# Kernel tuning notes

Measured on AMD Instinct MI355X. Metric: run time of the kernel, lower is better.

## Reference

```python
import jax, jax.numpy as jnp
import numpy as np

N_NODES = 50000
N_EDGES = 800000
IN_F = 256
HID = 64          # hidden_features; GAT layers output 2*HID = 128
OUT_F = 2
NUM_GRAPHS = 32
NEG_SLOPE = 0.2   # PyG GATConv default


def setup_inputs() -> dict:
    key = jax.random.key(0)
    ks = jax.random.split(key, 16)
    g = 2 * HID
    def glorot(k, shape):
        fan_in = shape[0] if len(shape) > 1 else shape[0]
        return jax.random.normal(k, shape, dtype=jnp.float32) / np.sqrt(fan_in)
    return {
        "x": jax.random.normal(ks[0], (N_NODES, IN_F), dtype=jnp.float32),
        "edge_index": jax.random.randint(ks[1], (2, N_EDGES), 0, N_NODES, dtype=jnp.int64),
        "batch": jnp.sort(jax.random.randint(ks[2], (N_NODES,), 0, NUM_GRAPHS, dtype=jnp.int64)),
        "W1": glorot(ks[3], (IN_F, g)),
        "as1": glorot(ks[4], (g,)),
        "ad1": glorot(ks[5], (g,)),
        "b1": jnp.zeros((g,), jnp.float32),
        "W2": glorot(ks[6], (g, g)),
        "as2": glorot(ks[7], (g,)),
        "ad2": glorot(ks[8], (g,)),
        "b2": jnp.zeros((g,), jnp.float32),
        "lw1": glorot(ks[9], (g, HID)),
        "lb1": jnp.zeros((HID,), jnp.float32),
        "lw2": glorot(ks[10], (HID, OUT_F)),
        "lb2": jnp.zeros((OUT_F,), jnp.float32),
    }


def _gat_conv(x, W, a_src, a_dst, bias, src, dst, n):
    # Single-head PyG GATConv: linear -> per-edge LeakyReLU attention logits ->
    # softmax over incoming edges per destination -> weighted scatter-sum.
    h = x @ W                                   # [N, F]
    es = h @ a_src                              # [N] source attention terms
    ed = h @ a_dst                              # [N] destination attention terms
    e = jax.nn.leaky_relu(es[src] + ed[dst], NEG_SLOPE)   # [E]
    m = jax.ops.segment_max(e, dst, num_segments=n)
    m = jnp.where(jnp.isfinite(m), m, 0.0)      # guard empty segments
    ex = jnp.exp(e - m[dst])
    den = jax.ops.segment_sum(ex, dst, num_segments=n)
    alpha = ex / (den[dst] + 1e-16)             # PyG softmax epsilon
    out = jax.ops.segment_sum(alpha[:, None] * h[src], dst, num_segments=n)
    return out + bias


def reference(x, edge_index, batch, W1, as1, ad1, b1, W2, as2, ad2, b2, lw1, lb1, lw2, lb2):
    n = x.shape[0]
    loops = jnp.arange(n, dtype=edge_index.dtype)
    src = jnp.concatenate([edge_index[0], loops])   # add_self_loops=True (PyG default)
    dst = jnp.concatenate([edge_index[1], loops])

    h = jax.nn.selu(_gat_conv(x, W1, as1, ad1, b1, src, dst, n))
    h = jax.nn.selu(_gat_conv(h, W2, as2, ad2, b2, src, dst, n))

    # global_mean_pool over graph-batch vector
    sums = jax.ops.segment_sum(h, batch, num_segments=NUM_GRAPHS)
    cnts = jax.ops.segment_sum(jnp.ones((n,), h.dtype), batch, num_segments=NUM_GRAPHS)
    pooled = sums / jnp.maximum(cnts, 1.0)[:, None]     # [B, 2*HID]

    z = jax.nn.selu(pooled)
    z = jax.nn.selu(z @ lw1 + lb1)
    z = z @ lw2 + lb2
    return jax.nn.log_softmax(z, axis=-1)
```

## Files before the change

kernel.cpp:

```cpp
#include <hip/hip_runtime.h>
#include <hip/hip_bf16.h>
#include <math.h>

#define N_NODES 50000
#define N_EDGES 800000
#define ET (N_EDGES + N_NODES)
#define IN_F 256
#define G 128
#define NHID 64
#define NGRAPH 32
#define NBUCK ((N_NODES + 255) / 256)
#define CAP 8192
#define POOL_NODES 64
#define EPB 4096
#define NBA ((ET + EPB - 1) / EPB)

typedef __hip_bfloat16 bf16;
typedef unsigned short ushort;
typedef __attribute__((ext_vector_type(8))) short short8;
typedef __attribute__((ext_vector_type(4))) float f32x4;

__device__ __forceinline__ float bf2f(ushort u) {
    union { unsigned u; float f; } c; c.u = ((unsigned)u) << 16; return c.f;
}
__device__ __forceinline__ ushort f2bf(float f) {
    unsigned u = __float_as_uint(f);
    u += 0x7FFFu + ((u >> 16) & 1u);
    return (ushort)(u >> 16);
}
__device__ __forceinline__ float ldf(const void* p, long i, int f32) {
    return f32 ? ((const float*)p)[i] : bf2f(((const ushort*)p)[i]);
}
__device__ __forceinline__ int ldi(const void* p, long i, int i64) {
    return i64 ? (int)((const long long*)p)[i] : ((const int*)p)[i];
}

__device__ __forceinline__ float selu_f(float x) {
    const float sc = 1.0507009873554805f, al = 1.6732632423543772f;
    return x > 0.f ? sc * x : sc * al * expm1f(x);
}

typedef const __attribute__((address_space(1))) void gas_void;
typedef __attribute__((address_space(3))) void las_void;
__device__ __forceinline__ void stage16(const void* g, void* l) {
    __builtin_amdgcn_global_load_lds((gas_void*)g, (las_void*)l, 16, 0, 0);
}

__global__ void detect_kernel(const void* x, const void* ei, int* flags,
                              int* bcur, float* gsum, float* gcnt) {
    int l = threadIdx.x;
    for (int k = l; k < NBUCK; k += 64) bcur[k] = 0;
    for (int k = l; k < NGRAPH * G; k += 64) gsum[k] = 0.f;
    if (l < NGRAPH) gcnt[l] = 0.f;
    const unsigned* xu = (const unsigned*)x;
    const long NW = (long)N_NODES * IN_F / 2;
    long stride = NW / 1024;
    int sane = 0;
    for (int k = l; k < 1024; k += 64) {
        unsigned u = xu[(long)k * stride];
        unsigned e = (u >> 23) & 0xFF;
        if (u == 0u || (e >= 100 && e <= 140)) sane++;
    }
    const unsigned* wu = (const unsigned*)ei;
    int nz = 0;
    for (int k = l; k < 1024; k += 64) {
        long j = ((long)k * 1562) | 1;
        nz += (wu[j] != 0u);
    }
    for (int off = 32; off; off >>= 1) {
        sane += __shfl_xor(sane, off);
        nz   += __shfl_xor(nz, off);
    }
    if (l == 0) {
        flags[0] = (sane >= 512) ? 1 : 0;
        flags[1] = (nz < 16) ? 1 : 0;
    }
}

__device__ __forceinline__ void edge_sd(const void* __restrict__ ei, int e, int i64,
                                        int& s, int& d) {
    if (e < N_EDGES) {
        s = ldi(ei, e, i64);
        d = ldi(ei, (long)N_EDGES + e, i64);
        s = min(max(s, 0), N_NODES - 1);
        d = min(max(d, 0), N_NODES - 1);
    } else {
        s = d = e - N_EDGES;
    }
}


__global__ __launch_bounds__(256) void binA_kernel(
    const void* __restrict__ ei, int* __restrict__ bcur, unsigned* __restrict__ pairs,
    const int* __restrict__ flags) {
    __shared__ int cnt[256], lofs[256], pcur[256], gbase[256];
    __shared__ unsigned stage[EPB];
    int t = threadIdx.x;
    int e0 = blockIdx.x * EPB;
    int nE = min(EPB, ET - e0);
    int i64 = flags[1];
    int sj[EPB / 256], dj[EPB / 256];
    cnt[t] = 0;
    __syncthreads();
#pragma unroll
    for (int j = 0; j < EPB / 256; j++) {
        int idx = j * 256 + t;
        if (idx < nE) {
            edge_sd(ei, e0 + idx, i64, sj[j], dj[j]);
            atomicAdd(&cnt[dj[j] >> 8], 1);
        } else dj[j] = -1;
    }
    __syncthreads();
    lofs[t] = cnt[t];
    for (int off = 1; off < 256; off <<= 1) {
        __syncthreads();
        int v = (t >= off) ? lofs[t - off] : 0;
        __syncthreads();
        lofs[t] += v;
    }
    __syncthreads();
    int excl = lofs[t] - cnt[t];
    __syncthreads();
    lofs[t] = excl;
    pcur[t] = excl;
    __syncthreads();
    if (t < NBUCK && cnt[t]) gbase[t] = atomicAdd(&bcur[t], cnt[t]);
    __syncthreads();
#pragma unroll
    for (int j = 0; j < EPB / 256; j++) {
        if (dj[j] >= 0) {
            int b = dj[j] >> 8;
            int lp = atomicAdd(&pcur[b], 1);
            stage[lp] = (unsigned)sj[j] | ((unsigned)(dj[j] & 255) << 16) |
                        ((unsigned)b << 24);
        }
    }
    __syncthreads();
    for (int i = t; i < nE; i += 256) {
        unsigned p = stage[i];
        int b = p >> 24;
        int idx = gbase[b] + i - lofs[b];
        if (idx < CAP)
            pairs[(size_t)b * CAP + idx] = p;
    }
}

__global__ __launch_bounds__(256) void binB_kernel(
    const unsigned* __restrict__ pairs, const int* __restrict__ bcur,
    int2* __restrict__ rowse, ushort* __restrict__ srcs) {
    __shared__ int cnt[256], cur[256];
    int b = blockIdx.x, t = threadIdx.x;
    int base = b * CAP;
    int n = min(bcur[b], CAP);
    cnt[t] = 0;
    __syncthreads();
    for (int i = t; i < n; i += 256)
        atomicAdd(&cnt[(pairs[base + i] >> 16) & 255], 1);
    __syncthreads();
    cur[t] = cnt[t];
    for (int off = 1; off < 256; off <<= 1) {
        __syncthreads();
        int v = (t >= off) ? cur[t - off] : 0;
        __syncthreads();
        cur[t] += v;
    }
    __syncthreads();
    int excl = cur[t] - cnt[t];
    __syncthreads();
    cur[t] = base + excl;
    int node = b * 256 + t;
    if (node < N_NODES) rowse[node] = make_int2(base + excl, base + excl + cnt[t]);
    __syncthreads();
    for (int i = t; i < n; i += 256) {
        unsigned p = pairs[base + i];
        int pos = atomicAdd(&cur[(p >> 16) & 255], 1);
        srcs[pos] = (ushort)(p & 0xFFFFu);
    }
}

__global__ void wt_kernel(const void* __restrict__ W1, const void* __restrict__ W2,
                          ushort* __restrict__ wt1, ushort* __restrict__ wt2,
                          const int* __restrict__ flags) {
    int i = blockIdx.x * 256 + threadIdx.x;
    int f32 = flags[0];
    const void* W; ushort* wt; int idx;
    if (i < IN_F * G) { W = W1; wt = wt1; idx = i; }
    else if (i < IN_F * G + G * G) { W = W2; wt = wt2; idx = i - IN_F * G; }
    else return;
    int k = idx >> 7, n = idx & (G - 1);
    float w = ldf(W, idx, f32);
    ushort h = f2bf(w);
    ushort lo = f2bf(w - bf2f(h));
    int c = k >> 5, q = (k >> 3) & 3, j = k & 7;
    int nt = n >> 4, n16 = n & 15;
    int lane = q * 16 + n16;
    size_t base = ((size_t)c * 16 + nt * 2) * 512 + lane * 8 + j;
    wt[base] = h;
    wt[base + 512] = lo;
}

template <int K, bool AF32>
__device__ __forceinline__ void gemm_body(
    const void* __restrict__ A, const ushort* __restrict__ wt,
    unsigned* __restrict__ H2, const int* __restrict__ flags,
    const void* __restrict__ aS, const void* __restrict__ aD,
    float2* __restrict__ es2, short8* sB8) {
    constexpr int NC = K / 32;
    int wave = threadIdx.x >> 6, lane = threadIdx.x & 63;
    int quad = lane >> 4, n16 = lane & 15;
    int rb = blockIdx.x * 64 + wave * 16;
    int rowa = min(rb + n16, N_NODES - 1);
    f32x4 acc[8];
#pragma unroll
    for (int t = 0; t < 8; t++) acc[t] = (f32x4){0.f, 0.f, 0.f, 0.f};

    for (int c = 0; c < NC; c++) {
#pragma unroll
        for (int i = 0; i < 4; i++) {
            int fw = wave * 4 + i;
            stage16(wt + ((size_t)c * 16 + fw) * 512 + lane * 8, &sB8[fw * 64]);
        }
        float av[8];
        if (AF32) {
            const float* ap = (const float*)A + (size_t)rowa * K + c * 32 + quad * 8;
            f32x4 a0 = *(const f32x4*)ap;
            f32x4 a1 = *(const f32x4*)(ap + 4);
#pragma unroll
            for (int j = 0; j < 4; j++) { av[j] = a0[j]; av[j + 4] = a1[j]; }
        } else {
            const ushort* ap = (const ushort*)A + (size_t)rowa * K + c * 32 + quad * 8;
#pragma unroll
            for (int j = 0; j < 8; j++) av[j] = bf2f(ap[j]);
        }
        short8 ahi, alo;
#pragma unroll
        for (int j = 0; j < 8; j++) {
            ushort h = f2bf(av[j]);
            ahi[j] = (short)h;
            alo[j] = (short)f2bf(av[j] - bf2f(h));
        }
        __syncthreads();
#pragma unroll
        for (int nt = 0; nt < 8; nt++) {
            short8 bh = sB8[(nt * 2 + 0) * 64 + lane];
            short8 bl = sB8[(nt * 2 + 1) * 64 + lane];
            acc[nt] = __builtin_amdgcn_mfma_f32_16x16x32_bf16(ahi, bh, acc[nt], 0, 0, 0);
            acc[nt] = __builtin_amdgcn_mfma_f32_16x16x32_bf16(ahi, bl, acc[nt], 0, 0, 0);
            acc[nt] = __builtin_amdgcn_mfma_f32_16x16x32_bf16(alo, bh, acc[nt], 0, 0, 0);
        }
        __syncthreads();
    }

    int f32 = flags[0];
    float asv[8], adv[8];
#pragma unroll
    for (int nt = 0; nt < 8; nt++) {
        asv[nt] = ldf(aS, nt * 16 + n16, f32);
        adv[nt] = ldf(aD, nt * 16 + n16, f32);
    }
#pragma unroll
    for (int r = 0; r < 4; r++) {
        int ro = rb + quad * 4 + r;
        float s = 0.f, dv = 0.f;
#pragma unroll
        for (int nt = 0; nt < 8; nt++) {
            s += acc[nt][r] * asv[nt];
            dv += acc[nt][r] * adv[nt];
        }
        if (ro < N_NODES) {
#pragma unroll
            for (int nt = 0; nt < 4; nt++) {
                unsigned pack = (unsigned)f2bf(acc[nt][r]) |
                                ((unsigned)f2bf(acc[nt + 4][r]) << 16);
                H2[(size_t)ro * 64 + nt * 16 + n16] = pack;
            }
        }
#pragma unroll
        for (int off = 8; off; off >>= 1) {
            s += __shfl_xor(s, off);
            dv += __shfl_xor(dv, off);
        }
        if (n16 == 0 && ro < N_NODES) es2[ro] = make_float2(s, dv);
    }
}

template <int K>
__global__ __launch_bounds__(256, 3) void gemm_mfma_kernel(
    const void* __restrict__ A, const ushort* __restrict__ wt,
    unsigned* __restrict__ H2, int a_mode, const int* __restrict__ flags,
    const void* __restrict__ aS, const void* __restrict__ aD,
    float2* __restrict__ es2) {
    __shared__ short8 sB8[16 * 64];
    int af32 = (a_mode == 2) ? 0 : flags[0];
    if (af32) gemm_body<K, true>(A, wt, H2, flags, aS, aD, es2, sB8);
    else      gemm_body<K, false>(A, wt, H2, flags, aS, aD, es2, sB8);
}

__global__ __launch_bounds__(256) void gat_agg_kernel(
    const unsigned* __restrict__ h2, const int2* __restrict__ rowse,
    const ushort* __restrict__ srcs, const float2* __restrict__ es2,
    const void* __restrict__ bias, ushort* __restrict__ outb,
    const int* __restrict__ flags) {
    int node = blockIdx.x * 4 + (threadIdx.x >> 6);
    if (node >= N_NODES) return;
    int l = threadIdx.x & 63;
    int2 se = rowse[node];
    int start = se.x, end = se.y;
    float edd = es2[node].y;
    float m = -INFINITY, den = 0.f;
    float acc0 = 0.f, acc1 = 0.f;
    for (int c0 = start; c0 < end; c0 += 64) {
        int cn = min(end - c0, 64);
        int s = 0; float v = -INFINITY;
        if (l < cn) {
            s = (int)srcs[c0 + l];
            v = es2[s].x + edd;
            v = v >= 0.f ? v : 0.2f * v;
        }
        float mc = v;
#pragma unroll
        for (int off = 32; off; off >>= 1) mc = fmaxf(mc, __shfl_xor(mc, off));
        float mnew = fmaxf(m, mc);
        float scale = expf(m - mnew);
        float p = (l < cn) ? expf(v - mnew) : 0.f;
        float lsum = p;
#pragma unroll
        for (int off = 32; off; off >>= 1) lsum += __shfl_xor(lsum, off);
        den = den * scale + lsum;
        acc0 *= scale; acc1 *= scale;
        int cnr = (cn + 7) & ~7;
        for (int i = 0; i < cnr; i += 8) {
            int sis[8]; float pis[8]; unsigned hv[8];
#pragma unroll
            for (int j = 0; j < 8; j++) {
                sis[j] = __builtin_amdgcn_readlane(s, i + j);
                pis[j] = __uint_as_float(
                    __builtin_amdgcn_readlane(__float_as_uint(p), i + j));
            }
#pragma unroll
            for (int j = 0; j < 8; j++)
                hv[j] = h2[(size_t)sis[j] * 64 + l];
#pragma unroll
            for (int j = 0; j < 8; j++) {
                acc0 += pis[j] * bf2f((ushort)(hv[j] & 0xFFFFu));
                acc1 += pis[j] * bf2f((ushort)(hv[j] >> 16));
            }
        }
        m = mnew;
    }
    float inv = 1.f / (den + 1e-16f);
    int f32 = flags[0];
    float o0 = acc0 * inv + ldf(bias, l, f32);
    float o1 = acc1 * inv + ldf(bias, l + 64, f32);
    outb[(size_t)node * G + l]      = f2bf(selu_f(o0));
    outb[(size_t)node * G + l + 64] = f2bf(selu_f(o1));
}

__global__ void pool_kernel(const ushort* __restrict__ h, const void* __restrict__ batch,
                            float* __restrict__ gsum, float* __restrict__ gcnt,
                            const int* __restrict__ flags) {
    int t = threadIdx.x;
    int i64 = flags[1];
    int i0 = blockIdx.x * POOL_NODES;
    int i1 = min(N_NODES, i0 + POOL_NODES);
    int cur = -1, runLen = 0;
    float acc = 0.f;
    for (int i = i0; i < i1; i++) {
        int g = min(max(ldi(batch, i, i64), 0), NGRAPH - 1);
        if (g != cur) {
            if (cur >= 0) {
                atomicAdd(&gsum[cur * G + t], acc);
                if (t == 0) atomicAdd(&gcnt[cur], (float)runLen);
            }
            cur = g; acc = 0.f; runLen = 0;
        }
        acc += bf2f(h[(size_t)i * G + t]);
        runLen++;
    }
    if (cur >= 0) {
        atomicAdd(&gsum[cur * G + t], acc);
        if (t == 0) atomicAdd(&gcnt[cur], (float)runLen);
    }
}

__global__ void head_kernel(const float* __restrict__ gsum, const float* __restrict__ gcnt,
                            const void* __restrict__ lw1, const void* __restrict__ lb1,
                            const void* __restrict__ lw2, const void* __restrict__ lb2,
                            float* __restrict__ out, const int* __restrict__ flags) {
    int g = blockIdx.x, t = threadIdx.x;
    int f32 = flags[0];
    __shared__ float z[G];
    __shared__ float z1[NHID];
    __shared__ float z2[2];
    float cnt = fmaxf(gcnt[g], 1.0f);
    z[t]      = selu_f(gsum[g * G + t] / cnt);
    z[t + 64] = selu_f(gsum[g * G + 64 + t] / cnt);
    __syncthreads();
    float a = ldf(lb1, t, f32);
    for (int k = 0; k < G; k++) a += z[k] * ldf(lw1, k * NHID + t, f32);
    z1[t] = selu_f(a);
    __syncthreads();
    if (t < 2) {
        float s = ldf(lb2, t, f32);
        for (int j = 0; j < NHID; j++) s += z1[j] * ldf(lw2, j * 2 + t, f32);
        z2[t] = s;
    }
    __syncthreads();
    if (t == 0) {
        float mx = fmaxf(z2[0], z2[1]);
        float l = mx + logf(expf(z2[0] - mx) + expf(z2[1] - mx));
        out[g * 2 + 0] = z2[0] - l;
        out[g * 2 + 1] = z2[1] - l;
    }
}

extern "C" void kernel_launch(void* const* d_in, const int* in_sizes, int n_in,
                              void* d_out, int out_size, void* d_ws, size_t ws_size,
                              hipStream_t stream) {
    const void* x    = d_in[0];
    const void* ei   = d_in[1];
    const void* batch= d_in[2];
    const void* W1   = d_in[3];
    const void* as1  = d_in[4];
    const void* ad1  = d_in[5];
    const void* b1   = d_in[6];
    const void* W2   = d_in[7];
    const void* as2  = d_in[8];
    const void* ad2  = d_in[9];
    const void* b2   = d_in[10];
    const void* lw1  = d_in[11];
    const void* lb1  = d_in[12];
    const void* lw2  = d_in[13];
    const void* lb2  = d_in[14];
    float* out = (float*)d_out;

    char* w = (char*)d_ws;
    size_t off = 0;
    auto alloc = [&](size_t bytes) -> char* {
        char* p = w + off;
        off = (off + bytes + 255) & ~(size_t)255;
        return p;
    };
    int*      flags  = (int*)alloc(256);
    unsigned* h2     = (unsigned*)alloc((size_t)N_NODES * 64 * 4);
    ushort*   abuf   = (ushort*)alloc((size_t)N_NODES * G * 2);
    float2*   es2    = (float2*)alloc((size_t)N_NODES * 8);
    int2*     rowse  = (int2*)alloc((size_t)N_NODES * 8);
    int*      bcur   = (int*)alloc((size_t)NBUCK * 4);
    unsigned* pairs  = (unsigned*)alloc((size_t)NBUCK * CAP * 4);
    ushort*   srcs   = (ushort*)alloc((size_t)NBUCK * CAP * 2);
    float*    gsum   = (float*)alloc((size_t)NGRAPH * G * 4);
    float*    gcnt   = (float*)alloc((size_t)NGRAPH * 4);
    ushort*   wt1    = (ushort*)alloc((size_t)IN_F * G * 2 * 2);
    ushort*   wt2    = (ushort*)alloc((size_t)G * G * 2 * 2);

    unsigned gemm_grid = (N_NODES + 63) / 64;
    unsigned agg_grid = (N_NODES + 3) / 4;

    detect_kernel<<<1, 64, 0, stream>>>(x, ei, flags, bcur, gsum, gcnt);

    binA_kernel<<<NBA, 256, 0, stream>>>(ei, bcur, pairs, flags);
    binB_kernel<<<NBUCK, 256, 0, stream>>>(pairs, bcur, rowse, srcs);

    wt_kernel<<<(IN_F * G + G * G + 255) / 256, 256, 0, stream>>>(W1, W2, wt1, wt2, flags);

    gemm_mfma_kernel<IN_F><<<gemm_grid, 256, 0, stream>>>(x, wt1, h2,
                                                          0, flags, as1, ad1, es2);
    gat_agg_kernel<<<agg_grid, 256, 0, stream>>>(h2, rowse, srcs, es2, b1, abuf, flags);

    gemm_mfma_kernel<G><<<gemm_grid, 256, 0, stream>>>(abuf, wt2, h2,
                                                       2, flags, as2, ad2, es2);
    gat_agg_kernel<<<agg_grid, 256, 0, stream>>>(h2, rowse, srcs, es2, b2, abuf, flags);

    pool_kernel<<<(N_NODES + POOL_NODES - 1) / POOL_NODES, 128, 0, stream>>>(
        abuf, batch, gsum, gcnt, flags);
    head_kernel<<<NGRAPH, 64, 0, stream>>>(gsum, gcnt, lw1, lb1, lw2, lb2, out, flags);
}
```

Measured before the change: 294.6 us.

## Fuse preprocessing kernels, merge binning with GEMM, and fold pooling into aggregation

Result: slower. 339.3 us (+15.2%).

```diff
diff --git a/kernel.cpp b/kernel.cpp
--- a/kernel.cpp
+++ b/kernel.cpp
@@ -10,8 +10,8 @@
 #define NHID 64
 #define NGRAPH 32
 #define NBUCK ((N_NODES + 255) / 256)
-#define CAP 8192
-#define POOL_NODES 64
+#define CAPB 8192
+#define CELL 64
 #define EPB 4096
 #define NBA ((ET + EPB - 1) / EPB)
 
@@ -44,37 +44,6 @@
 typedef __attribute__((address_space(3))) void las_void;
 __device__ __forceinline__ void stage16(const void* g, void* l) {
     __builtin_amdgcn_global_load_lds((gas_void*)g, (las_void*)l, 16, 0, 0);
-}
-
-__global__ void detect_kernel(const void* x, const void* ei, int* flags,
-                              int* bcur, float* gsum, float* gcnt) {
-    int l = threadIdx.x;
-    for (int k = l; k < NBUCK; k += 64) bcur[k] = 0;
-    for (int k = l; k < NGRAPH * G; k += 64) gsum[k] = 0.f;
-    if (l < NGRAPH) gcnt[l] = 0.f;
-    const unsigned* xu = (const unsigned*)x;
-    const long NW = (long)N_NODES * IN_F / 2;
-    long stride = NW / 1024;
-    int sane = 0;
-    for (int k = l; k < 1024; k += 64) {
-        unsigned u = xu[(long)k * stride];
-        unsigned e = (u >> 23) & 0xFF;
-        if (u == 0u || (e >= 100 && e <= 140)) sane++;
-    }
-    const unsigned* wu = (const unsigned*)ei;
-    int nz = 0;
-    for (int k = l; k < 1024; k += 64) {
-        long j = ((long)k * 1562) | 1;
-        nz += (wu[j] != 0u);
-    }
-    for (int off = 32; off; off >>= 1) {
-        sane += __shfl_xor(sane, off);
-        nz   += __shfl_xor(nz, off);
-    }
-    if (l == 0) {
-        flags[0] = (sane >= 512) ? 1 : 0;
-        flags[1] = (nz < 16) ? 1 : 0;
-    }
 }
 
 __device__ __forceinline__ void edge_sd(const void* __restrict__ ei, int e, int i64,
@@ -91,17 +60,36 @@
 
 
 __global__ __launch_bounds__(256) void binA_kernel(
-    const void* __restrict__ ei, int* __restrict__ bcur, unsigned* __restrict__ pairs,
-    const int* __restrict__ flags) {
-    __shared__ int cnt[256], lofs[256], pcur[256], gbase[256];
+    const void* __restrict__ ei, unsigned* __restrict__ pairs,
+    int* __restrict__ cnts, int* __restrict__ flags,
+    const void* __restrict__ x,
+    const void* __restrict__ W1, const void* __restrict__ W2,
+    ushort* __restrict__ wt1, ushort* __restrict__ wt2) {
+    __shared__ int cnt[256], lofs[256], pcur[256];
     __shared__ unsigned stage[EPB];
+    __shared__ int s_i64, s_f32;
     int t = threadIdx.x;
+
+    if (t < 64) {
+        const unsigned* wu = (const unsigned*)ei;
+        long j = 1 + (long)t * 24986;
+        unsigned long long bal = __ballot(wu[j] != 0u);
+        if (t == 0) s_i64 = (__popcll(bal) < 16) ? 1 : 0;
+    } else if (t < 128) {
+        const unsigned* xu = (const unsigned*)x;
+        unsigned u = xu[(long)(t - 64) * 100000];
+        unsigned e = (u >> 23) & 0xFF;
+        unsigned long long bal = __ballot(u == 0u || (e >= 100 && e <= 140));
+        if (t == 64) s_f32 = (__popcll(bal) >= 32) ? 1 : 0;
+    }
+    cnt[t] = 0;
+    __syncthreads();
+    int i64 = s_i64, f32 = s_f32;
+    if (blockIdx.x == 0 && t == 0) { flags[0] = f32; flags[1] = i64; }
+
     int e0 = blockIdx.x * EPB;
     int nE = min(EPB, ET - e0);
-    int i64 = flags[1];
     int sj[EPB / 256], dj[EPB / 256];
-    cnt[t] = 0;
-    __syncthreads();
 #pragma unroll
     for (int j = 0; j < EPB / 256; j++) {
         int idx = j * 256 + t;
@@ -124,8 +112,6 @@
     lofs[t] = excl;
     pcur[t] = excl;
     __syncthreads();
-    if (t < NBUCK && cnt[t]) gbase[t] = atomicAdd(&bcur[t], cnt[t]);
-    __syncthreads();
 #pragma unroll
     for (int j = 0; j < EPB / 256; j++) {
         if (dj[j] >= 0) {
@@ -139,23 +125,49 @@
     for (int i = t; i < nE; i += 256) {
         unsigned p = stage[i];
         int b = p >> 24;
-        int idx = gbase[b] + i - lofs[b];
-        if (idx < CAP)
-            pairs[(size_t)b * CAP + idx] = p;
-    }
-}
-
-__global__ __launch_bounds__(256) void binB_kernel(
-    const unsigned* __restrict__ pairs, const int* __restrict__ bcur,
-    int2* __restrict__ rowse, ushort* __restrict__ srcs) {
-    __shared__ int cnt[256], cur[256];
-    int b = blockIdx.x, t = threadIdx.x;
-    int base = b * CAP;
-    int n = min(bcur[b], CAP);
+        int off2 = i - lofs[b];
+        if (off2 < CELL)
+            pairs[((size_t)b * NBA + blockIdx.x) * CELL + off2] = p;
+    }
+    if (t < NBUCK) cnts[(size_t)t * NBA + blockIdx.x] = min(cnt[t], CELL);
+
+    int wi = blockIdx.x * 256 + t;
+    if (wi < IN_F * G + G * G) {
+        const void* W; ushort* wtp; int idx;
+        if (wi < IN_F * G) { W = W1; wtp = wt1; idx = wi; }
+        else { W = W2; wtp = wt2; idx = wi - IN_F * G; }
+        int k = idx >> 7, n = idx & (G - 1);
+        float wv = ldf(W, idx, f32);
+        ushort h = f2bf(wv);
+        ushort lo = f2bf(wv - bf2f(h));
+        int c = k >> 5, q = (k >> 3) & 3, j = k & 7;
+        int nt = n >> 4, n16 = n & 15;
+        int lane = q * 16 + n16;
+        size_t base = ((size_t)c * 16 + nt * 2) * 512 + lane * 8 + j;
+        wtp[base] = h;
+        wtp[base + 512] = lo;
+    }
+}
+
+__device__ __forceinline__ void binB_body(
+    const unsigned* __restrict__ pairs, const int* __restrict__ cnts,
+    int2* __restrict__ rowse, ushort* __restrict__ srcs,
+    int b, int t, int* cnt, int* cur, int* ccnt) {
+    if (t < NBA) ccnt[t] = cnts[(size_t)b * NBA + t];
     cnt[t] = 0;
     __syncthreads();
-    for (int i = t; i < n; i += 256)
-        atomicAdd(&cnt[(pairs[base + i] >> 16) & 255], 1);
+    if (t < NBA) {
+        const unsigned* cp = pairs + ((size_t)b * NBA + t) * CELL;
+        int n = ccnt[t], i = 0;
+        for (; i + 4 <= n; i += 4) {
+            unsigned r0 = cp[i], r1 = cp[i + 1], r2 = cp[i + 2], r3 = cp[i + 3];
+            atomicAdd(&cnt[(r0 >> 16) & 255], 1);
+            atomicAdd(&cnt[(r1 >> 16) & 255], 1);
+            atomicAdd(&cnt[(r2 >> 16) & 255], 1);
+            atomicAdd(&cnt[(r3 >> 16) & 255], 1);
+        }
+        for (; i < n; i++) atomicAdd(&cnt[(cp[i] >> 16) & 255], 1);
+    }
     __syncthreads();
     cur[t] = cnt[t];
     for (int off = 1; off < 256; off <<= 1) {
@@ -164,51 +176,45 @@
         __syncthreads();
         cur[t] += v;
     }
-    __syncthreads();
     int excl = cur[t] - cnt[t];
+    int base = b * CAPB;
     __syncthreads();
     cur[t] = base + excl;
     int node = b * 256 + t;
     if (node < N_NODES) rowse[node] = make_int2(base + excl, base + excl + cnt[t]);
     __syncthreads();
-    for (int i = t; i < n; i += 256) {
-        unsigned p = pairs[base + i];
-        int pos = atomicAdd(&cur[(p >> 16) & 255], 1);
-        srcs[pos] = (ushort)(p & 0xFFFFu);
-    }
-}
-
-__global__ void wt_kernel(const void* __restrict__ W1, const void* __restrict__ W2,
-                          ushort* __restrict__ wt1, ushort* __restrict__ wt2,
-                          const int* __restrict__ flags) {
-    int i = blockIdx.x * 256 + threadIdx.x;
-    int f32 = flags[0];
-    const void* W; ushort* wt; int idx;
-    if (i < IN_F * G) { W = W1; wt = wt1; idx = i; }
-    else if (i < IN_F * G + G * G) { W = W2; wt = wt2; idx = i - IN_F * G; }
-    else return;
-    int k = idx >> 7, n = idx & (G - 1);
-    float w = ldf(W, idx, f32);
-    ushort h = f2bf(w);
-    ushort lo = f2bf(w - bf2f(h));
-    int c = k >> 5, q = (k >> 3) & 3, j = k & 7;
-    int nt = n >> 4, n16 = n & 15;
-    int lane = q * 16 + n16;
-    size_t base = ((size_t)c * 16 + nt * 2) * 512 + lane * 8 + j;
-    wt[base] = h;
-    wt[base + 512] = lo;
+    if (t < NBA) {
+        const unsigned* cp = pairs + ((size_t)b * NBA + t) * CELL;
+        int n = ccnt[t], i = 0;
+        for (; i + 4 <= n; i += 4) {
+            unsigned r0 = cp[i], r1 = cp[i + 1], r2 = cp[i + 2], r3 = cp[i + 3];
+            int p0 = atomicAdd(&cur[(r0 >> 16) & 255], 1);
+            int p1 = atomicAdd(&cur[(r1 >> 16) & 255], 1);
+            int p2 = atomicAdd(&cur[(r2 >> 16) & 255], 1);
+            int p3 = atomicAdd(&cur[(r3 >> 16) & 255], 1);
+            srcs[p0] = (ushort)(r0 & 0xFFFFu);
+            srcs[p1] = (ushort)(r1 & 0xFFFFu);
+            srcs[p2] = (ushort)(r2 & 0xFFFFu);
+            srcs[p3] = (ushort)(r3 & 0xFFFFu);
+        }
+        for (; i < n; i++) {
+            unsigned r = cp[i];
+            int p = atomicAdd(&cur[(r >> 16) & 255], 1);
+            srcs[p] = (ushort)(r & 0xFFFFu);
+        }
+    }
 }
 
 template <int K, bool AF32>
 __device__ __forceinline__ void gemm_body(
-    const void* __restrict__ A, const ushort* __restrict__ wt,
+    int bid, const void* __restrict__ A, const ushort* __restrict__ wt,
     unsigned* __restrict__ H2, const int* __restrict__ flags,
     const void* __restrict__ aS, const void* __restrict__ aD,
     float2* __restrict__ es2, short8* sB8) {
     constexpr int NC = K / 32;
     int wave = threadIdx.x >> 6, lane = threadIdx.x & 63;
     int quad = lane >> 4, n16 = lane & 15;
-    int rb = blockIdx.x * 64 + wave * 16;
+    int rb = bid * 64 + wave * 16;
     int rowa = min(rb + n16, N_NODES - 1);
     f32x4 acc[8];
 #pragma unroll
@@ -285,21 +291,45 @@
 }
 
 template <int K>
+__global__ __launch_bounds__(256, 3) void binB_gemm_kernel(
+    const unsigned* __restrict__ pairs, const int* __restrict__ cnts,
+    int2* __restrict__ rowse, ushort* __restrict__ srcs,
+    const void* __restrict__ A, const ushort* __restrict__ wt,
+    unsigned* __restrict__ H2, const int* __restrict__ flags,
+    const void* __restrict__ aS, const void* __restrict__ aD,
+    float2* __restrict__ es2) {
+    __shared__ short8 sB8[16 * 64];
+    __shared__ int s_cnt[256], s_cur[256], s_ccnt[NBA];
+    if (blockIdx.x < NBUCK) {
+        binB_body(pairs, cnts, rowse, srcs, blockIdx.x, threadIdx.x,
+                  s_cnt, s_cur, s_ccnt);
+        return;
+    }
+    int bid = blockIdx.x - NBUCK;
+    if (flags[0]) gemm_body<K, true>(bid, A, wt, H2, flags, aS, aD, es2, sB8);
+    else          gemm_body<K, false>(bid, A, wt, H2, flags, aS, aD, es2, sB8);
+}
+
+template <int K>
 __global__ __launch_bounds__(256, 3) void gemm_mfma_kernel(
     const void* __restrict__ A, const ushort* __restrict__ wt,
     unsigned* __restrict__ H2, int a_mode, const int* __restrict__ flags,
     const void* __restrict__ aS, const void* __restrict__ aD,
-    float2* __restrict__ es2) {
+    float2* __restrict__ es2, float* __restrict__ zbuf) {
     __shared__ short8 sB8[16 * 64];
+    if (zbuf != nullptr && blockIdx.x == 0) {
+        for (int i = threadIdx.x; i < NGRAPH * G; i += 256) zbuf[i] = 0.f;
+    }
     int af32 = (a_mode == 2) ? 0 : flags[0];
-    if (af32) gemm_body<K, true>(A, wt, H2, flags, aS, aD, es2, sB8);
-    else      gemm_body<K, false>(A, wt, H2, flags, aS, aD, es2, sB8);
+    if (af32) gemm_body<K, true>(blockIdx.x, A, wt, H2, flags, aS, aD, es2, sB8);
+    else      gemm_body<K, false>(blockIdx.x, A, wt, H2, flags, aS, aD, es2, sB8);
 }
 
 __global__ __launch_bounds__(256) void gat_agg_kernel(
     const unsigned* __restrict__ h2, const int2* __restrict__ rowse,
     const ushort* __restrict__ srcs, const float2* __restrict__ es2,
     const void* __restrict__ bias, ushort* __restrict__ outb,
+    const void* __restrict__ batch, float* __restrict__ gsum, int pool,
     const int* __restrict__ flags) {
     int node = blockIdx.x * 4 + (threadIdx.x >> 6);
     if (node >= N_NODES) return;
@@ -350,49 +380,40 @@
     }
     float inv = 1.f / (den + 1e-16f);
     int f32 = flags[0];
-    float o0 = acc0 * inv + ldf(bias, l, f32);
-    float o1 = acc1 * inv + ldf(bias, l + 64, f32);
-    outb[(size_t)node * G + l]      = f2bf(selu_f(o0));
-    outb[(size_t)node * G + l + 64] = f2bf(selu_f(o1));
-}
-
-__global__ void pool_kernel(const ushort* __restrict__ h, const void* __restrict__ batch,
-                            float* __restrict__ gsum, float* __restrict__ gcnt,
-                            const int* __restrict__ flags) {
-    int t = threadIdx.x;
-    int i64 = flags[1];
-    int i0 = blockIdx.x * POOL_NODES;
-    int i1 = min(N_NODES, i0 + POOL_NODES);
-    int cur = -1, runLen = 0;
-    float acc = 0.f;
-    for (int i = i0; i < i1; i++) {
-        int g = min(max(ldi(batch, i, i64), 0), NGRAPH - 1);
-        if (g != cur) {
-            if (cur >= 0) {
-                atomicAdd(&gsum[cur * G + t], acc);
-                if (t == 0) atomicAdd(&gcnt[cur], (float)runLen);
-            }
-            cur = g; acc = 0.f; runLen = 0;
-        }
-        acc += bf2f(h[(size_t)i * G + t]);
-        runLen++;
-    }
-    if (cur >= 0) {
-        atomicAdd(&gsum[cur * G + t], acc);
-        if (t == 0) atomicAdd(&gcnt[cur], (float)runLen);
-    }
-}
-
-__global__ void head_kernel(const float* __restrict__ gsum, const float* __restrict__ gcnt,
+    float o0 = selu_f(acc0 * inv + ldf(bias, l, f32));
+    float o1 = selu_f(acc1 * inv + ldf(bias, l + 64, f32));
+    if (pool) {
+        int gid = min(max(ldi(batch, node, flags[1]), 0), NGRAPH - 1);
+        atomicAdd(&gsum[gid * G + l], o0);
+        atomicAdd(&gsum[gid * G + 64 + l], o1);
+    } else {
+        outb[(size_t)node * G + l]      = f2bf(o0);
+        outb[(size_t)node * G + l + 64] = f2bf(o1);
+    }
+}
+
+__global__ void head_kernel(const float* __restrict__ gsum, const void* __restrict__ batch,
                             const void* __restrict__ lw1, const void* __restrict__ lb1,
                             const void* __restrict__ lw2, const void* __restrict__ lb2,
                             float* __restrict__ out, const int* __restrict__ flags) {
     int g = blockIdx.x, t = threadIdx.x;
-    int f32 = flags[0];
+    int f32 = flags[0], i64 = flags[1];
     __shared__ float z[G];
     __shared__ float z1[NHID];
     __shared__ float z2[2];
-    float cnt = fmaxf(gcnt[g], 1.0f);
+    __shared__ int sb[2];
+    if (t < 2) {
+        int target = g + t;
+        int lo = 0, hi = N_NODES;
+        while (lo < hi) {
+            int mid = (lo + hi) >> 1;
+            int v = ldi(batch, mid, i64);
+            if (v < target) lo = mid + 1; else hi = mid;
+        }
+        sb[t] = lo;
+    }
+    __syncthreads();
+    float cnt = fmaxf((float)(sb[1] - sb[0]), 1.0f);
     z[t]      = selu_f(gsum[g * G + t] / cnt);
     z[t + 64] = selu_f(gsum[g * G + 64 + t] / cnt);
     __syncthreads();
@@ -446,33 +467,24 @@
     ushort*   abuf   = (ushort*)alloc((size_t)N_NODES * G * 2);
     float2*   es2    = (float2*)alloc((size_t)N_NODES * 8);
     int2*     rowse  = (int2*)alloc((size_t)N_NODES * 8);
-    int*      bcur   = (int*)alloc((size_t)NBUCK * 4);
-    unsigned* pairs  = (unsigned*)alloc((size_t)NBUCK * CAP * 4);
-    ushort*   srcs   = (ushort*)alloc((size_t)NBUCK * CAP * 2);
+    unsigned* pairs  = (unsigned*)alloc((size_t)NBUCK * NBA * CELL * 4);
+    int*      cnts   = (int*)alloc((size_t)NBUCK * NBA * 4);
+    ushort*   srcs   = (ushort*)alloc((size_t)NBUCK * CAPB * 2);
     float*    gsum   = (float*)alloc((size_t)NGRAPH * G * 4);
-    float*    gcnt   = (float*)alloc((size_t)NGRAPH * 4);
     ushort*   wt1    = (ushort*)alloc((size_t)IN_F * G * 2 * 2);
     ushort*   wt2    = (ushort*)alloc((size_t)G * G * 2 * 2);
 
     unsigned gemm_grid = (N_NODES + 63) / 64;
     unsigned agg_grid = (N_NODES + 3) / 4;
 
-    detect_kernel<<<1, 64, 0, stream>>>(x, ei, flags, bcur, gsum, gcnt);
-
-    binA_kernel<<<NBA, 256, 0, stream>>>(ei, bcur, pairs, flags);
-    binB_kernel<<<NBUCK, 256, 0, stream>>>(pairs, bcur, rowse, srcs);
-
-    wt_kernel<<<(IN_F * G + G * G + 255) / 256, 256, 0, stream>>>(W1, W2, wt1, wt2, flags);
-
-    gemm_mfma_kernel<IN_F><<<gemm_grid, 256, 0, stream>>>(x, wt1, h2,
-                                                          0, flags, as1, ad1, es2);
-    gat_agg_kernel<<<agg_grid, 256, 0, stream>>>(h2, rowse, srcs, es2, b1, abuf, flags);
-
-    gemm_mfma_kernel<G><<<gemm_grid, 256, 0, stream>>>(abuf, wt2, h2,
-                                                       2, flags, as2, ad2, es2);
-    gat_agg_kernel<<<agg_grid, 256, 0, stream>>>(h2, rowse, srcs, es2, b2, abuf, flags);
-
-    pool_kernel<<<(N_NODES + POOL_NODES - 1) / POOL_NODES, 128, 0, stream>>>(
-        abuf, batch, gsum, gcnt, flags);
-    head_kernel<<<NGRAPH, 64, 0, stream>>>(gsum, gcnt, lw1, lb1, lw2, lb2, out, flags);
-}
+    binA_kernel<<<NBA, 256, 0, stream>>>(ei, pairs, cnts, flags, x, W1, W2, wt1, wt2);
+    binB_gemm_kernel<IN_F><<<NBUCK + gemm_grid, 256, 0, stream>>>(
+        pairs, cnts, rowse, srcs, x, wt1, h2, flags, as1, ad1, es2);
+    gat_agg_kernel<<<agg_grid, 256, 0, stream>>>(h2, rowse, srcs, es2, b1, abuf,
+                                                 nullptr, nullptr, 0, flags);
+    gemm_mfma_kernel<G><<<gemm_grid, 256, 0, stream>>>(abuf, wt2, h2, 2, flags,
+                                                       as2, ad2, es2, gsum);
+    gat_agg_kernel<<<agg_grid, 256, 0, stream>>>(h2, rowse, srcs, es2, b2, nullptr,
+                                                 batch, gsum, 1, flags);
+    head_kernel<<<NGRAPH, 64, 0, stream>>>(gsum, batch, lw1, lb1, lw2, lb2, out, flags);
+}
```
